# Kernel optimization log

Hardware: AMD Instinct MI355X
Metric: run time of the kernel (lower is better)

Reference implementation:

```python
import jax, jax.numpy as jnp
import numpy as np

B, L, C, Kf = 32, 4096, 64, 4
MAX_FREQ_RATIO = 0.2
NAN_FRAC = 0.15


def setup_inputs() -> dict:
    key = jax.random.key(0)
    k1, k2, k3, k4 = jax.random.split(key, 4)
    x = jax.random.normal(k1, (B, L, C), dtype=jnp.float32)
    # inject missing values (the module is built around NaN handling)
    nan_mask = jax.random.uniform(k2, (B, L, C)) < NAN_FRAC
    x = jnp.where(nan_mask, jnp.nan, x)
    freq_len = L // 2 + 1
    max_thr = max(1, int(freq_len * MAX_FREQ_RATIO))  # 409
    taus = jax.random.randint(k3, (Kf,), 1, max_thr + 1, dtype=jnp.int32)
    mus = jax.random.randint(k4, (Kf,), 0, 2, dtype=jnp.int32)
    return {"x": x, "taus": taus, "mus": mus}


def _fill_missing(x):
    """Vectorized forward-fill then backward-fill of NaNs along time axis.
    Matches the GPU branch of linear_interpolate_missing: NaN -> last observed
    value; leading NaNs -> next observed value; all-NaN series -> 0."""
    Bb, Ll, Cc = x.shape
    obs = ~jnp.isnan(x)                                  # [B,L,C]
    ar = jnp.arange(Ll)[None, :, None]
    # index of most recent observed position (-1 if none yet)
    ff = jax.lax.cummax(jnp.where(obs, ar, -1), axis=1)
    # index of next observed position (L if none ahead)
    bf = jnp.flip(jax.lax.cummin(jnp.flip(jnp.where(obs, ar, Ll), 1), axis=1), 1)
    xz = jnp.where(obs, x, 0.0)                          # NaN-safe gather source
    v_ff = jnp.take_along_axis(xz, jnp.clip(ff, 0, Ll - 1), axis=1)
    v_bf = jnp.take_along_axis(xz, jnp.clip(bf, 0, Ll - 1), axis=1)
    return jnp.where(obs, x,
                     jnp.where(ff >= 0, v_ff,
                               jnp.where(bf < Ll, v_bf, 0.0)))


def reference(x, taus, mus):
    Bb, Ll, Cc = x.shape
    x_clean = _fill_missing(x)                           # [B,L,C]
    xf = jnp.fft.rfft(x_clean, axis=1)                   # [B,F,C] complex64, F=L//2+1
    fidx = jnp.arange(xf.shape[1])                       # [F]
    # mu==1: zero out [tau:] (keep low freqs); mu==0: zero out [:tau] (keep high)
    keep = jnp.where(mus[:, None] == 1,
                     fidx[None, :] < taus[:, None],
                     fidx[None, :] >= taus[:, None])     # [Kf,F] bool
    masked = xf[None, :, :, :] * keep[:, None, :, None].astype(xf.dtype)
    out = jnp.fft.irfft(masked, n=Ll, axis=2)            # [Kf,B,L,C] float32
    return out
```

## Files before the change

kernel.cpp:

```cpp
#include <hip/hip_runtime.h>
#include <math.h>


namespace {

constexpr int NFFT = 4096;
constexpr int NT   = 256;
constexpr int NB   = 32;
constexpr int NC   = 64;
constexpr int KF   = 4;

typedef __fp16 h2 __attribute__((ext_vector_type(2)));

__device__ __forceinline__ int pad(int i) { return i + (i >> 4); }

__device__ __forceinline__ unsigned packh(float x, float y){
    h2 h = __builtin_amdgcn_cvt_pkrtz(x, y);
    return __builtin_bit_cast(unsigned, h);
}
__device__ __forceinline__ float2 unpackh(unsigned u){
    h2 h = __builtin_bit_cast(h2, u);
    return make_float2((float)h.x, (float)h.y);
}

__device__ __forceinline__ float2 cadd(float2 a, float2 b){ return make_float2(a.x+b.x, a.y+b.y); }
__device__ __forceinline__ float2 csub(float2 a, float2 b){ return make_float2(a.x-b.x, a.y-b.y); }
__device__ __forceinline__ float2 cmul(float2 a, float2 b){
    return make_float2(fmaf(a.x,b.x,-(a.y*b.y)), fmaf(a.x,b.y, a.y*b.x));
}
__device__ __forceinline__ float2 cmulc(float2 a, float2 b){
    return make_float2(fmaf(a.x,b.x, a.y*b.y), fmaf(a.y,b.x,-(a.x*b.y)));
}

__device__ __forceinline__ void bf4_fwd(float2&a,float2&b,float2&c,float2&d){
    float2 t0=cadd(a,c), t1=csub(a,c), t2=cadd(b,d), t3=csub(b,d);
    float2 mi3=make_float2(t3.y,-t3.x);
    a=cadd(t0,t2); b=cadd(t1,mi3); c=csub(t0,t2); d=csub(t1,mi3);
}
__device__ __forceinline__ void bf4_inv(float2&a,float2&b,float2&c,float2&d){
    float2 t0=cadd(a,c), t1=csub(a,c), t2=cadd(b,d), t3=csub(b,d);
    float2 pi3=make_float2(-t3.y,t3.x);
    a=cadd(t0,t2); b=cadd(t1,pi3); c=csub(t0,t2); d=csub(t1,pi3);
}
__device__ __forceinline__ void grp_fwd(float2&a,float2&b,float2&c,float2&d,
                                        float2 w1, float2 w2, float2 w3){
    bf4_fwd(a,b,c,d);
    b=cmul(b,w1); c=cmul(c,w2); d=cmul(d,w3);
}
__device__ __forceinline__ void xgrp_fwd(float2&a,float2&b,float2&c,float2&d, float2 w1){
    float2 w2=cmul(w1,w1), w3=cmul(w2,w1);
    grp_fwd(a,b,c,d,w1,w2,w3);
}
__device__ __forceinline__ void grp_inv(float2&a,float2&b,float2&c,float2&d,
                                        float2 w1, float2 w2, float2 w3){
    b=cmulc(b,w1); c=cmulc(c,w2); d=cmulc(d,w3);
    bf4_inv(a,b,c,d);
}
__device__ __forceinline__ void xgrp_inv(float2&a,float2&b,float2&c,float2&d, float2 w1){
    float2 w2=cmul(w1,w1), w3=cmul(w2,w1);
    grp_inv(a,b,c,d,w1,w2,w3);
}

__global__ __launch_bounds__(NT)
void dfl_kernel(const float* __restrict__ x,
                const int* __restrict__ taus,
                const int* __restrict__ mus,
                float* __restrict__ out)
{
    __shared__ unsigned bufh[NFFT + NFFT/16];
    __shared__ unsigned spech[NFFT + NFFT/16];
    __shared__ float2 wtab[512];

    const int tid = threadIdx.x;
    const int l  = ((blockIdx.x & 7) << 7) | (blockIdx.x >> 3);
    const int b  = l >> 5;
    const int c0 = (l & 31) << 1;
    const float QNAN = __uint_as_float(0x7fc00000u);

    for (int j = tid; j < 512; j += NT) {
        float s, c; sincosf(-3.14159265358979f * (float)j / 2048.0f, &s, &c);
        wtab[j] = make_float2(c, s);
    }

    float2* chLast  = reinterpret_cast<float2*>(spech);
    float2* chFirst = reinterpret_cast<float2*>(spech) + 256;

    const float* xb = x + ((size_t)b * NFFT) * NC + c0;
    float2 z[16];
    float2 last = make_float2(QNAN, QNAN), first = make_float2(QNAN, QNAN);
    #pragma unroll
    for (int j = 0; j < 16; ++j) {
        float2 v = *reinterpret_cast<const float2*>(xb + (size_t)(16*tid + j) * NC);
        if (first.x != first.x && v.x == v.x) first.x = v.x;
        if (first.y != first.y && v.y == v.y) first.y = v.y;
        if (v.x == v.x) last.x = v.x; else v.x = last.x;
        if (v.y == v.y) last.y = v.y; else v.y = last.y;
        z[j] = v;
    }
    chLast[tid] = last;
    chFirst[tid] = first;
    __syncthreads();

    float2 pre = make_float2(QNAN, QNAN);
    for (int kk = tid - 1; kk >= 0; --kk) {
        float2 s2 = chLast[kk];
        if (pre.x != pre.x) pre.x = s2.x;
        if (pre.y != pre.y) pre.y = s2.y;
        if (pre.x == pre.x && pre.y == pre.y) break;
    }
    float2 gfirst = make_float2(QNAN, QNAN);
    for (int kk = 0; kk < NT; ++kk) {
        float2 s2 = chFirst[kk];
        if (gfirst.x != gfirst.x) gfirst.x = s2.x;
        if (gfirst.y != gfirst.y) gfirst.y = s2.y;
        if (gfirst.x == gfirst.x && gfirst.y == gfirst.y) break;
    }
    if (gfirst.x != gfirst.x) gfirst.x = 0.f;
    if (gfirst.y != gfirst.y) gfirst.y = 0.f;
    const float fx = (pre.x == pre.x) ? pre.x : gfirst.x;
    const float fy = (pre.y == pre.y) ? pre.y : gfirst.y;
    const float scale = 1.0f / (float)NFFT;
    #pragma unroll
    for (int j = 0; j < 16; ++j) {
        if (z[j].x != z[j].x) z[j].x = fx;
        if (z[j].y != z[j].y) z[j].y = fy;
        z[j].x *= scale; z[j].y *= scale;
    }

    const float2 wm = wtab[tid];
    float2 q2 = cmul(wm, wm);
    const float2 w4m = cmul(q2, q2);
    const float2 w16r = wtab[16 * (tid & 15)];
    float2 q3 = cmul(w16r, w16r);
    const float2 w64r = cmul(q3, q3);

    const float2 W1 = make_float2( 0.92387953251f,-0.38268343236f);
    const float2 W2 = make_float2( 0.70710678119f,-0.70710678119f);
    const float2 W3 = make_float2( 0.38268343236f,-0.92387953251f);
    const float2 W4 = make_float2( 0.f,-1.f);
    const float2 W6 = make_float2(-0.70710678119f,-0.70710678119f);
    const float2 W9 = make_float2(-0.92387953251f, 0.38268343236f);

    __syncthreads();

    #pragma unroll
    for (int j = 0; j < 16; ++j) bufh[pad(16*tid + j)] = packh(z[j].x, z[j].y);
    __syncthreads();

    #pragma unroll
    for (int j = 0; j < 16; ++j) z[j] = unpackh(bufh[pad(tid + 256*j)]);
    xgrp_fwd(z[0],z[4],z[8],z[12], wm);
    xgrp_fwd(z[1],z[5],z[9],z[13], cmul(wm,W1));
    xgrp_fwd(z[2],z[6],z[10],z[14], cmul(wm,W2));
    xgrp_fwd(z[3],z[7],z[11],z[15], cmul(wm,W3));
    {   float2 w1=w4m, w2=cmul(w1,w1), w3=cmul(w2,w1);
        grp_fwd(z[0],z[1],z[2],z[3],  w1,w2,w3);
        grp_fwd(z[4],z[5],z[6],z[7],  w1,w2,w3);
        grp_fwd(z[8],z[9],z[10],z[11],w1,w2,w3);
        grp_fwd(z[12],z[13],z[14],z[15],w1,w2,w3);
    }
    #pragma unroll
    for (int j = 0; j < 16; ++j) bufh[pad(tid + 256*j)] = packh(z[j].x, z[j].y);
    __syncthreads();

    const int p2b = ((tid >> 4) << 8) + (tid & 15);
    #pragma unroll
    for (int j = 0; j < 16; ++j) z[j] = unpackh(bufh[pad(p2b + 16*j)]);
    xgrp_fwd(z[0],z[4],z[8],z[12], w16r);
    xgrp_fwd(z[1],z[5],z[9],z[13], cmul(w16r,W1));
    xgrp_fwd(z[2],z[6],z[10],z[14], cmul(w16r,W2));
    xgrp_fwd(z[3],z[7],z[11],z[15], cmul(w16r,W3));
    {   float2 w1=w64r, w2=cmul(w1,w1), w3=cmul(w2,w1);
        grp_fwd(z[0],z[1],z[2],z[3],  w1,w2,w3);
        grp_fwd(z[4],z[5],z[6],z[7],  w1,w2,w3);
        grp_fwd(z[8],z[9],z[10],z[11],w1,w2,w3);
        grp_fwd(z[12],z[13],z[14],z[15],w1,w2,w3);
    }
    #pragma unroll
    for (int j = 0; j < 16; ++j) bufh[pad(p2b + 16*j)] = packh(z[j].x, z[j].y);
    __syncthreads();

    #pragma unroll
    for (int j = 0; j < 16; ++j) z[j] = unpackh(bufh[pad(16*tid + j)]);
    bf4_fwd(z[0],z[4],z[8],z[12]);
    grp_fwd(z[1],z[5],z[9],z[13], W1,W2,W3);
    grp_fwd(z[2],z[6],z[10],z[14], W2,W4,W6);
    grp_fwd(z[3],z[7],z[11],z[15], W3,W6,W9);
    bf4_fwd(z[0],z[1],z[2],z[3]);
    bf4_fwd(z[4],z[5],z[6],z[7]);
    bf4_fwd(z[8],z[9],z[10],z[11]);
    bf4_fwd(z[12],z[13],z[14],z[15]);

    #pragma unroll
    for (int j = 0; j < 16; ++j) spech[pad(16*tid + j)] = packh(z[j].x, z[j].y);

    const int revtid = ((tid & 3) << 6) | (((tid >> 2) & 3) << 4)
                     | (((tid >> 4) & 3) << 2) | (tid >> 6);

    #pragma unroll 1
    for (int k = 0; k < KF; ++k) {
        const int tau = taus[k];
        const int mu  = mus[k];
        __syncthreads();

        #pragma unroll
        for (int j = 0; j < 16; ++j) {
            const int r = revtid + ((j & 3) << 10) + ((j >> 2) << 8);
            const int f = (r <= 2048) ? r : (NFFT - r);
            const bool keep = (mu == 1) ? (f < tau) : (f >= tau);
            z[j] = keep ? unpackh(spech[pad(16*tid + j)]) : make_float2(0.f, 0.f);
        }
        bf4_inv(z[0],z[1],z[2],z[3]);
        bf4_inv(z[4],z[5],z[6],z[7]);
        bf4_inv(z[8],z[9],z[10],z[11]);
        bf4_inv(z[12],z[13],z[14],z[15]);
        bf4_inv(z[0],z[4],z[8],z[12]);
        grp_inv(z[1],z[5],z[9],z[13], W1,W2,W3);
        grp_inv(z[2],z[6],z[10],z[14], W2,W4,W6);
        grp_inv(z[3],z[7],z[11],z[15], W3,W6,W9);
        #pragma unroll
        for (int j = 0; j < 16; ++j) bufh[pad(16*tid + j)] = packh(z[j].x, z[j].y);
        __syncthreads();

        #pragma unroll
        for (int j = 0; j < 16; ++j) z[j] = unpackh(bufh[pad(p2b + 16*j)]);
        {   float2 w1=w64r, w2=cmul(w1,w1), w3=cmul(w2,w1);
            grp_inv(z[0],z[1],z[2],z[3],  w1,w2,w3);
            grp_inv(z[4],z[5],z[6],z[7],  w1,w2,w3);
            grp_inv(z[8],z[9],z[10],z[11],w1,w2,w3);
            grp_inv(z[12],z[13],z[14],z[15],w1,w2,w3);
        }
        xgrp_inv(z[0],z[4],z[8],z[12], w16r);
        xgrp_inv(z[1],z[5],z[9],z[13], cmul(w16r,W1));
        xgrp_inv(z[2],z[6],z[10],z[14], cmul(w16r,W2));
        xgrp_inv(z[3],z[7],z[11],z[15], cmul(w16r,W3));
        #pragma unroll
        for (int j = 0; j < 16; ++j) bufh[pad(p2b + 16*j)] = packh(z[j].x, z[j].y);
        __syncthreads();

        #pragma unroll
        for (int j = 0; j < 16; ++j) z[j] = unpackh(bufh[pad(tid + 256*j)]);
        {   float2 w1=w4m, w2=cmul(w1,w1), w3=cmul(w2,w1);
            grp_inv(z[0],z[1],z[2],z[3],  w1,w2,w3);
            grp_inv(z[4],z[5],z[6],z[7],  w1,w2,w3);
            grp_inv(z[8],z[9],z[10],z[11],w1,w2,w3);
            grp_inv(z[12],z[13],z[14],z[15],w1,w2,w3);
        }
        xgrp_inv(z[0],z[4],z[8],z[12], wm);
        xgrp_inv(z[1],z[5],z[9],z[13], cmul(wm,W1));
        xgrp_inv(z[2],z[6],z[10],z[14], cmul(wm,W2));
        xgrp_inv(z[3],z[7],z[11],z[15], cmul(wm,W3));

        float* ob = out + ((size_t)(k*NB + b) * NFFT) * NC + c0;
        #pragma unroll
        for (int j = 0; j < 16; ++j) {
            const int t = tid + 256*j;
            *reinterpret_cast<float2*>(ob + (size_t)t * NC) = z[j];
        }
    }
}

}

extern "C" void kernel_launch(void* const* d_in, const int* in_sizes, int n_in,
                              void* d_out, int out_size, void* d_ws, size_t ws_size,
                              hipStream_t stream) {
    (void)in_sizes; (void)n_in; (void)out_size; (void)d_ws; (void)ws_size;
    const float* x  = (const float*)d_in[0];
    const int* taus = (const int*)d_in[1];
    const int* mus  = (const int*)d_in[2];
    float* out      = (float*)d_out;
    dfl_kernel<<<dim3(NB * NC / 2), dim3(NT), 0, stream>>>(x, taus, mus, out);
}
```

Measured before the change: 102.0 us.

## Split fused kernel into forward FFT and per-filter inverse FFT kernels

The single kernel, which ran the forward FFT and then looped over the four filters serially in one block, is split into two launches. The forward kernel writes the fp16-packed spectrum to the workspace. The inverse kernel launches four times as many blocks, one per (filter, batch, channel-pair), so the inverse FFTs run in parallel across more blocks. This trades an extra launch plus a workspace write and read of the spectrum for higher parallelism and smaller shared memory per block.

```diff
diff --git a/kernel.cpp b/kernel.cpp
--- a/kernel.cpp
+++ b/kernel.cpp
@@ -62,13 +62,9 @@
 }
 
 __global__ __launch_bounds__(NT)
-void dfl_kernel(const float* __restrict__ x,
-                const int* __restrict__ taus,
-                const int* __restrict__ mus,
-                float* __restrict__ out)
+void dfl_fwd(const float* __restrict__ x, unsigned* __restrict__ ws)
 {
     __shared__ unsigned bufh[NFFT + NFFT/16];
-    __shared__ unsigned spech[NFFT + NFFT/16];
     __shared__ float2 wtab[512];
 
     const int tid = threadIdx.x;
@@ -82,8 +78,8 @@
         wtab[j] = make_float2(c, s);
     }
 
-    float2* chLast  = reinterpret_cast<float2*>(spech);
-    float2* chFirst = reinterpret_cast<float2*>(spech) + 256;
+    float2* chLast  = reinterpret_cast<float2*>(bufh);
+    float2* chFirst = reinterpret_cast<float2*>(bufh) + 256;
 
     const float* xb = x + ((size_t)b * NFFT) * NC + c0;
     float2 z[16];
@@ -191,72 +187,121 @@
     bf4_fwd(z[8],z[9],z[10],z[11]);
     bf4_fwd(z[12],z[13],z[14],z[15]);
 
-    #pragma unroll
-    for (int j = 0; j < 16; ++j) spech[pad(16*tid + j)] = packh(z[j].x, z[j].y);
+    uint4* w4 = reinterpret_cast<uint4*>(ws);
+    #pragma unroll
+    for (int q = 0; q < 4; ++q) {
+        w4[((size_t)l * 4 + q) * NT + tid] =
+            make_uint4(packh(z[4*q+0].x, z[4*q+0].y),
+                       packh(z[4*q+1].x, z[4*q+1].y),
+                       packh(z[4*q+2].x, z[4*q+2].y),
+                       packh(z[4*q+3].x, z[4*q+3].y));
+    }
+}
+
+__global__ __launch_bounds__(NT)
+void dfl_inv(const unsigned* __restrict__ ws,
+             const int* __restrict__ taus,
+             const int* __restrict__ mus,
+             float* __restrict__ out)
+{
+    __shared__ unsigned bufh[NFFT + NFFT/16];
+    __shared__ float2 wtab[512];
+
+    const int tid = threadIdx.x;
+    const int l2   = ((blockIdx.x & 7) << 9) | (blockIdx.x >> 3);
+    const int pair = l2 & 31;
+    const int kb   = l2 >> 5;
+    const int b    = kb & 31;
+    const int k    = kb >> 5;
+    const int c0   = pair << 1;
+    const int lsp  = (b << 5) | pair;
+
+    for (int j = tid; j < 512; j += NT) {
+        float s, c; sincosf(-3.14159265358979f * (float)j / 2048.0f, &s, &c);
+        wtab[j] = make_float2(c, s);
+    }
+
+    float2 z[16];
+    const uint4* w4 = reinterpret_cast<const uint4*>(ws);
+    #pragma unroll
+    for (int q = 0; q < 4; ++q) {
+        uint4 v = w4[((size_t)lsp * 4 + q) * NT + tid];
+        z[4*q+0] = unpackh(v.x); z[4*q+1] = unpackh(v.y);
+        z[4*q+2] = unpackh(v.z); z[4*q+3] = unpackh(v.w);
+    }
 
     const int revtid = ((tid & 3) << 6) | (((tid >> 2) & 3) << 4)
                      | (((tid >> 4) & 3) << 2) | (tid >> 6);
-
-    #pragma unroll 1
-    for (int k = 0; k < KF; ++k) {
-        const int tau = taus[k];
-        const int mu  = mus[k];
-        __syncthreads();
-
-        #pragma unroll
-        for (int j = 0; j < 16; ++j) {
-            const int r = revtid + ((j & 3) << 10) + ((j >> 2) << 8);
-            const int f = (r <= 2048) ? r : (NFFT - r);
-            const bool keep = (mu == 1) ? (f < tau) : (f >= tau);
-            z[j] = keep ? unpackh(spech[pad(16*tid + j)]) : make_float2(0.f, 0.f);
-        }
-        bf4_inv(z[0],z[1],z[2],z[3]);
-        bf4_inv(z[4],z[5],z[6],z[7]);
-        bf4_inv(z[8],z[9],z[10],z[11]);
-        bf4_inv(z[12],z[13],z[14],z[15]);
-        bf4_inv(z[0],z[4],z[8],z[12]);
-        grp_inv(z[1],z[5],z[9],z[13], W1,W2,W3);
-        grp_inv(z[2],z[6],z[10],z[14], W2,W4,W6);
-        grp_inv(z[3],z[7],z[11],z[15], W3,W6,W9);
-        #pragma unroll
-        for (int j = 0; j < 16; ++j) bufh[pad(16*tid + j)] = packh(z[j].x, z[j].y);
-        __syncthreads();
-
-        #pragma unroll
-        for (int j = 0; j < 16; ++j) z[j] = unpackh(bufh[pad(p2b + 16*j)]);
-        {   float2 w1=w64r, w2=cmul(w1,w1), w3=cmul(w2,w1);
-            grp_inv(z[0],z[1],z[2],z[3],  w1,w2,w3);
-            grp_inv(z[4],z[5],z[6],z[7],  w1,w2,w3);
-            grp_inv(z[8],z[9],z[10],z[11],w1,w2,w3);
-            grp_inv(z[12],z[13],z[14],z[15],w1,w2,w3);
-        }
+    const int tau = taus[k];
+    const int mu  = mus[k];
+    #pragma unroll
+    for (int j = 0; j < 16; ++j) {
+        const int r = revtid + ((j & 3) << 10) + ((j >> 2) << 8);
+        const int f = (r <= 2048) ? r : (NFFT - r);
+        const bool keep = (mu == 1) ? (f < tau) : (f >= tau);
+        if (!keep) z[j] = make_float2(0.f, 0.f);
+    }
+
+    const float2 W1 = make_float2( 0.92387953251f,-0.38268343236f);
+    const float2 W2 = make_float2( 0.70710678119f,-0.70710678119f);
+    const float2 W3 = make_float2( 0.38268343236f,-0.92387953251f);
+    const float2 W4 = make_float2( 0.f,-1.f);
+    const float2 W6 = make_float2(-0.70710678119f,-0.70710678119f);
+    const float2 W9 = make_float2(-0.92387953251f, 0.38268343236f);
+
+    bf4_inv(z[0],z[1],z[2],z[3]);
+    bf4_inv(z[4],z[5],z[6],z[7]);
+    bf4_inv(z[8],z[9],z[10],z[11]);
+    bf4_inv(z[12],z[13],z[14],z[15]);
+    bf4_inv(z[0],z[4],z[8],z[12]);
+    grp_inv(z[1],z[5],z[9],z[13], W1,W2,W3);
+    grp_inv(z[2],z[6],z[10],z[14], W2,W4,W6);
+    grp_inv(z[3],z[7],z[11],z[15], W3,W6,W9);
+    #pragma unroll
+    for (int j = 0; j < 16; ++j) bufh[pad(16*tid + j)] = packh(z[j].x, z[j].y);
+    __syncthreads();
+
+    const int p2b = ((tid >> 4) << 8) + (tid & 15);
+    #pragma unroll
+    for (int j = 0; j < 16; ++j) z[j] = unpackh(bufh[pad(p2b + 16*j)]);
+    {   const float2 w16r = wtab[16 * (tid & 15)];
+        float2 q3 = cmul(w16r, w16r);
+        float2 w1 = cmul(q3, q3);
+        float2 w2 = cmul(w1,w1), w3 = cmul(w2,w1);
+        grp_inv(z[0],z[1],z[2],z[3],  w1,w2,w3);
+        grp_inv(z[4],z[5],z[6],z[7],  w1,w2,w3);
+        grp_inv(z[8],z[9],z[10],z[11],w1,w2,w3);
+        grp_inv(z[12],z[13],z[14],z[15],w1,w2,w3);
         xgrp_inv(z[0],z[4],z[8],z[12], w16r);
         xgrp_inv(z[1],z[5],z[9],z[13], cmul(w16r,W1));
         xgrp_inv(z[2],z[6],z[10],z[14], cmul(w16r,W2));
         xgrp_inv(z[3],z[7],z[11],z[15], cmul(w16r,W3));
-        #pragma unroll
-        for (int j = 0; j < 16; ++j) bufh[pad(p2b + 16*j)] = packh(z[j].x, z[j].y);
-        __syncthreads();
-
-        #pragma unroll
-        for (int j = 0; j < 16; ++j) z[j] = unpackh(bufh[pad(tid + 256*j)]);
-        {   float2 w1=w4m, w2=cmul(w1,w1), w3=cmul(w2,w1);
-            grp_inv(z[0],z[1],z[2],z[3],  w1,w2,w3);
-            grp_inv(z[4],z[5],z[6],z[7],  w1,w2,w3);
-            grp_inv(z[8],z[9],z[10],z[11],w1,w2,w3);
-            grp_inv(z[12],z[13],z[14],z[15],w1,w2,w3);
-        }
+    }
+    #pragma unroll
+    for (int j = 0; j < 16; ++j) bufh[pad(p2b + 16*j)] = packh(z[j].x, z[j].y);
+    __syncthreads();
+
+    #pragma unroll
+    for (int j = 0; j < 16; ++j) z[j] = unpackh(bufh[pad(tid + 256*j)]);
+    {   const float2 wm = wtab[tid];
+        float2 q2 = cmul(wm, wm);
+        float2 w1 = cmul(q2, q2);
+        float2 w2 = cmul(w1,w1), w3 = cmul(w2,w1);
+        grp_inv(z[0],z[1],z[2],z[3],  w1,w2,w3);
+        grp_inv(z[4],z[5],z[6],z[7],  w1,w2,w3);
+        grp_inv(z[8],z[9],z[10],z[11],w1,w2,w3);
+        grp_inv(z[12],z[13],z[14],z[15],w1,w2,w3);
         xgrp_inv(z[0],z[4],z[8],z[12], wm);
         xgrp_inv(z[1],z[5],z[9],z[13], cmul(wm,W1));
         xgrp_inv(z[2],z[6],z[10],z[14], cmul(wm,W2));
         xgrp_inv(z[3],z[7],z[11],z[15], cmul(wm,W3));
-
-        float* ob = out + ((size_t)(k*NB + b) * NFFT) * NC + c0;
-        #pragma unroll
-        for (int j = 0; j < 16; ++j) {
-            const int t = tid + 256*j;
-            *reinterpret_cast<float2*>(ob + (size_t)t * NC) = z[j];
-        }
+    }
+
+    float* ob = out + ((size_t)(k*NB + b) * NFFT) * NC + c0;
+    #pragma unroll
+    for (int j = 0; j < 16; ++j) {
+        const int t = tid + 256*j;
+        *reinterpret_cast<float2*>(ob + (size_t)t * NC) = z[j];
     }
 }
 
@@ -265,10 +310,12 @@
 extern "C" void kernel_launch(void* const* d_in, const int* in_sizes, int n_in,
                               void* d_out, int out_size, void* d_ws, size_t ws_size,
                               hipStream_t stream) {
-    (void)in_sizes; (void)n_in; (void)out_size; (void)d_ws; (void)ws_size;
+    (void)in_sizes; (void)n_in; (void)out_size; (void)ws_size;
     const float* x  = (const float*)d_in[0];
     const int* taus = (const int*)d_in[1];
     const int* mus  = (const int*)d_in[2];
     float* out      = (float*)d_out;
-    dfl_kernel<<<dim3(NB * NC / 2), dim3(NT), 0, stream>>>(x, taus, mus, out);
-}
+    unsigned* ws    = (unsigned*)d_ws;
+    dfl_fwd<<<dim3(NB * NC / 2), dim3(NT), 0, stream>>>(x, ws);
+    dfl_inv<<<dim3(KF * NB * NC / 2), dim3(NT), 0, stream>>>(ws, taus, mus, out);
+}
```

Measured after the change: 113.1 us. +10.9%, slower.
